# Kernel optimization log

Measured on AMD Instinct MI355X. Metric: run time of the kernel, lower is better.

Reference implementation:

```python
import jax, jax.numpy as jnp
import numpy as np

N = 32768          # total nodes in batch (M graphs * N_agents)
E = N * 8          # edges (k_neighbors = 8)
DIN = 16           # node_obs_dim
DE = 8             # edge_dim (rel_pos 2 + one-hot 4 + dist 1 + payoff 1)
HE = 128           # embed_hidden_size
C = 64             # TransformerConv out_channels
H = 4              # heads (concat)
HC = H * C         # 256, final node embedding dim
EPS = 1e-5


def _ln(x, g, b):
    m = x.mean(-1, keepdims=True)
    v = ((x - m) ** 2).mean(-1, keepdims=True)
    return (x - m) * jax.lax.rsqrt(v + EPS) * g + b


def _seg_softmax(s, seg, n):
    # numerically stable softmax over edges grouped by destination node
    m = jax.ops.segment_max(s, seg, num_segments=n)
    e = jnp.exp(s - m[seg])
    z = jax.ops.segment_sum(e, seg, num_segments=n)
    return e / z[seg]


def setup_inputs() -> dict:
    key = jax.random.key(0)
    ks = jax.random.split(key, 40)

    def w(i, shape):
        return jax.random.normal(ks[i], shape, jnp.float32) * 0.05

    inp = {
        "x": jax.random.normal(ks[0], (N, DIN), jnp.float32),
        "edge_index": jax.random.randint(ks[1], (2, E), 0, N, dtype=jnp.int32),
        "edge_attr": jax.random.normal(ks[2], (E, DE), jnp.float32),
        # EmbedConv: lin1 + LN + one hidden Linear + LN (embed_layer_N=1)
        "e_W1": w(3, (DIN + DE, HE)), "e_b1": jnp.zeros((HE,), jnp.float32),
        "e_g1": jnp.ones((HE,), jnp.float32), "e_be1": jnp.zeros((HE,), jnp.float32),
        "e_W2": w(4, (HE, HE)), "e_b2": jnp.zeros((HE,), jnp.float32),
        "e_g2": jnp.ones((HE,), jnp.float32), "e_be2": jnp.zeros((HE,), jnp.float32),
    }
    # Two TransformerConv layers; layer0 in=HE, layer1 in=HC (concat heads)
    for l, din in enumerate([HE, HC]):
        base = 5 + l * 6
        inp[f"l{l}_Wq"] = w(base, (din, HC));     inp[f"l{l}_bq"] = jnp.zeros((HC,), jnp.float32)
        inp[f"l{l}_Wk"] = w(base + 1, (din, HC)); inp[f"l{l}_bk"] = jnp.zeros((HC,), jnp.float32)
        inp[f"l{l}_Wv"] = w(base + 2, (din, HC)); inp[f"l{l}_bv"] = jnp.zeros((HC,), jnp.float32)
        inp[f"l{l}_We"] = w(base + 3, (DE, HC))   # lin_edge has no bias in PyG
        inp[f"l{l}_Ws"] = w(base + 4, (din, HC)); inp[f"l{l}_bs"] = jnp.zeros((HC,), jnp.float32)
    return inp


def _tconv(h, edge_attr, src, dst, Wq, bq, Wk, bk, Wv, bv, We, Ws, bs):
    q = (h @ Wq + bq).reshape(N, H, C)
    k = (h @ Wk + bk).reshape(N, H, C)
    v = (h @ Wv + bv).reshape(N, H, C)
    e = (edge_attr @ We).reshape(E, H, C)
    ke = k[src] + e                      # [E,H,C]
    ve = v[src] + e                      # [E,H,C]
    s = (q[dst] * ke).sum(-1) / np.float32(np.sqrt(C))  # [E,H]
    a = _seg_softmax(s, dst, N)          # softmax over in-edges of each dst
    out = jax.ops.segment_sum(a[..., None] * ve, dst, num_segments=N)
    return out.reshape(N, HC) + h @ Ws + bs  # root_weight skip + bias


def reference(x, edge_attr, e_W1, e_b1, e_g1, e_be1, e_W2, e_b2, e_g2, e_be2,
              l0_Wq, l0_bq, l0_Wk, l0_bk, l0_Wv, l0_bv, l0_We, l0_Ws, l0_bs,
              l1_Wq, l1_bq, l1_Wk, l1_bk, l1_Wv, l1_bv, l1_We, l1_Ws, l1_bs,
              edge_index):
    src, dst = edge_index[0], edge_index[1]
    # EmbedConv: per-edge MLP on cat(x_j, edge_attr), scatter-add to dst
    m = jnp.concatenate([x[src], edge_attr], axis=1)    # [E, DIN+DE]
    m = _ln(jax.nn.relu(m @ e_W1 + e_b1), e_g1, e_be1)
    m = _ln(jax.nn.relu(m @ e_W2 + e_b2), e_g2, e_be2)
    h = jax.ops.segment_sum(m, dst, num_segments=N)      # [N, HE]
    # Two TransformerConv layers with ReLU activations
    h = jax.nn.relu(_tconv(h, edge_attr, src, dst, l0_Wq, l0_bq, l0_Wk, l0_bk,
                           l0_Wv, l0_bv, l0_We, l0_Ws, l0_bs))
    h = jax.nn.relu(_tconv(h, edge_attr, src, dst, l1_Wq, l1_bq, l1_Wk, l1_bk,
                           l1_Wv, l1_bv, l1_We, l1_Ws, l1_bs))
    return h  # graph_aggr == 'node': [N, HC]
```

## Files before the change

### kernel.cpp

```cpp
#include <hip/hip_runtime.h>
#include <hip/hip_bf16.h>

#define NN 32768
#define NE 262144

typedef unsigned short u16;
typedef unsigned int   u32;
typedef __bf16 bf16x8 __attribute__((ext_vector_type(8)));
typedef float  f32x16 __attribute__((ext_vector_type(16)));

__device__ __forceinline__ float bf2f(u16 u){ return __uint_as_float(((u32)u)<<16); }
__device__ __forceinline__ u16 f2bf(float f){ __hip_bfloat16 h = __float2bfloat16(f); return *(u16*)&h; }
__device__ __forceinline__ float4 ldbf4(const u16* p){
  ushort4 u = *(const ushort4*)p;
  return make_float4(bf2f(u.x), bf2f(u.y), bf2f(u.z), bf2f(u.w));
}
__device__ __forceinline__ void gload16(const void* g, void* l){
  __builtin_amdgcn_global_load_lds(
      (const __attribute__((address_space(1))) void*)g,
      (__attribute__((address_space(3))) void*)l, 16, 0, 0);
}

__global__ void k_deg(const int* __restrict__ ei, int* deg){
  int e = blockIdx.x*256 + threadIdx.x;
  if (e < NE) atomicAdd(&deg[ei[NE + e]], 1);
}

__global__ void k_scan1(const int* __restrict__ deg, int* __restrict__ rowptr, int* __restrict__ bsum){
  const int t = threadIdx.x, b = blockIdx.x;
  const int i = b*256 + t;
  const int ln = t & 63, wv = t >> 6;
  int v = deg[i];
  #pragma unroll
  for (int d = 1; d < 64; d <<= 1){
    int u = __shfl_up(v, d, 64);
    if (ln >= d) v += u;
  }
  __shared__ int wsum[4];
  if (ln == 63) wsum[wv] = v;
  __syncthreads();
  int p = 0;
  #pragma unroll
  for (int w = 0; w < 4; w++) if (w < wv) p += wsum[w];
  v += p;
  rowptr[i + 1] = v;
  if (t == 255) bsum[b] = v;
}

__global__ void k_scan2(const int* __restrict__ bsum, int* __restrict__ boff){
  const int t = threadIdx.x;
  const int ln = t & 63, wv = t >> 6;
  int own = bsum[t];
  int v = own;
  #pragma unroll
  for (int d = 1; d < 64; d <<= 1){
    int u = __shfl_up(v, d, 64);
    if (ln >= d) v += u;
  }
  __shared__ int wsum[2];
  if (ln == 63) wsum[wv] = v;
  __syncthreads();
  if (wv == 1) v += wsum[0];
  boff[t] = v - own;
}

__global__ void k_scan3(int* __restrict__ rowptr, const int* __restrict__ boff){
  const int t = threadIdx.x, b = blockIdx.x;
  rowptr[1 + b*256 + t] += boff[b];
  if (b == 0 && t == 0) rowptr[0] = 0;
}

__global__ void k_fill(const int* __restrict__ ei, const int* __restrict__ rowptr,
                       int* cursor, int* __restrict__ csrc, int* __restrict__ cedge){
  int e = blockIdx.x*256 + threadIdx.x;
  if (e < NE){
    int d = ei[NE + e];
    int p = rowptr[d] + atomicAdd(&cursor[d], 1);
    csrc[p]  = ei[e];
    cedge[p] = e;
  }
}

__global__ void k_b2p(const float* __restrict__ W2, const float* __restrict__ be1,
                      const float* __restrict__ b2, float* __restrict__ b2p){
  int f = threadIdx.x;
  float a = b2[f];
  for (int k = 0; k < 128; k++) a += be1[k]*W2[k*128 + f];
  b2p[f] = a;
}

__global__ void k_eprep(const float* __restrict__ W1, const float* __restrict__ b1,
                        const float* __restrict__ W2, const float* __restrict__ g1,
                        const float* __restrict__ b2p, __bf16* __restrict__ Ecat){
  int i = blockIdx.x*256 + threadIdx.x;
  if (i >= 2816) return;
  bf16x8 v;
  if (i < 512){
    int r = i & 31, hh = (i>>5)&1, ks = (i>>6)&1, rt = i>>7;
    int feat = rt*32 + r, k0 = ks*16 + hh*8;
    #pragma unroll
    for (int j = 0; j < 8; j++){
      int k = k0 + j;
      float val = (k < 24) ? W1[k*128 + feat] : ((k == 24) ? b1[feat] : 0.f);
      v[j] = (__bf16)val;
    }
  } else {
    int m = i - 512;
    int r = m & 31, hh = (m>>5)&1, q = m>>6;
    int ks = q % 9, rt = q / 9;
    int feat = rt*32 + r, k0 = ks*16 + hh*8;
    #pragma unroll
    for (int j = 0; j < 8; j++){
      int k = k0 + j;
      float val = (k < 128) ? g1[k]*W2[k*128 + feat] : ((k == 128) ? b2p[feat] : 0.f);
      v[j] = (__bf16)val;
    }
  }
  *(bf16x8*)&Ecat[(size_t)i*8] = v;
}

struct WPtrs { const float* w[8]; const float* b[8]; };

__global__ void k_wprep(WPtrs wp, __bf16* __restrict__ W0cat, __bf16* __restrict__ W1cat,
                        float* __restrict__ bcat0, float* __restrict__ bcat1){
  int gid = blockIdx.x*256 + threadIdx.x;
  if (gid < 16384){
    int mat = gid >> 12, v = gid & 4095;
    int colm = v & 255, q = v >> 8;
    int k0 = (q>>1)*16 + (q&1)*8;
    const float* W = wp.w[mat];
    bf16x8 vec;
    #pragma unroll
    for (int j = 0; j < 8; j++) vec[j] = (__bf16)W[(size_t)(k0+j)*256 + colm];
    *(bf16x8*)&W0cat[((size_t)q*1024 + mat*256 + colm)*8] = vec;
  } else if (gid < 49152){
    int g = gid - 16384;
    int mat = g >> 13, v = g & 8191;
    int colm = v & 255, q = v >> 8;
    int k0 = (q>>1)*16 + (q&1)*8;
    const float* W = wp.w[4+mat];
    bf16x8 vec;
    #pragma unroll
    for (int j = 0; j < 8; j++) vec[j] = (__bf16)W[(size_t)(k0+j)*256 + colm];
    *(bf16x8*)&W1cat[((size_t)q*1024 + mat*256 + colm)*8] = vec;
  } else if (gid < 51200){
    int g = gid - 49152;
    if (g < 1024) bcat0[g] = wp.b[g>>8][g&255];
    else { int h = g-1024; bcat1[h] = wp.b[4 + (h>>8)][h&255]; }
  }
}

__global__ __launch_bounds__(256, 1) void k_embed(
    const float* __restrict__ x, const float* __restrict__ ea,
    const int* __restrict__ csrc, const int* __restrict__ cedge, const int* __restrict__ rowptr,
    const __bf16* __restrict__ Ecat,
    const float* __restrict__ g2, const float* __restrict__ be2,
    u16* __restrict__ h0b)
{
  __shared__ alignas(16) __bf16 sE[2816*8];
  __shared__ float sg2[128], sbe2[128];
  const int t = threadIdx.x;
  const int wv = t >> 6, ln = t & 63, hi = ln >> 5, c32 = ln & 31;

  #pragma unroll
  for (int k = 0; k < 11; k++){
    int base = k*256 + wv*64;
    gload16(Ecat + (size_t)(base + ln)*8, &sE[(size_t)base*8]);
  }
  if (t < 128){ sg2[t] = g2[t]; sbe2[t] = be2[t]; }
  asm volatile("s_waitcnt vmcnt(0)" ::: "memory");
  __syncthreads();

  const int d   = (blockIdx.x*4 + wv)*32 + c32;
  const int rp  = rowptr[d];
  const int deg = rowptr[d+1] - rp;
  int md = deg;
  #pragma unroll
  for (int m = 1; m < 32; m <<= 1) md = max(md, __shfl_xor(md, m, 32));

  f32x16 hacc[4] = {};

  bool vc = deg > 0;
  int p0 = vc ? rp : 0;
  int sc = csrc[p0], ec = cedge[p0];
  float4 xa = *(const float4*)&x[(size_t)sc*16 + hi*8];
  float4 xb = *(const float4*)&x[(size_t)sc*16 + hi*8 + 4];
  float4 ga = *(const float4*)&ea[(size_t)ec*8];
  float4 gb = *(const float4*)&ea[(size_t)ec*8 + 4];

  for (int j = 0; j < md; j++){
    const float vm = vc ? 1.f : 0.f;
    bf16x8 b1f0, b1f1;
    {
      float xv[8]; *(float4*)&xv[0] = xa; *(float4*)&xv[4] = xb;
      #pragma unroll
      for (int q = 0; q < 8; q++) b1f0[q] = (__bf16)(xv[q]*vm);
      float evv[8]; *(float4*)&evv[0] = ga; *(float4*)&evv[4] = gb;
      #pragma unroll
      for (int q = 0; q < 8; q++)
        b1f1[q] = (__bf16)(hi ? ((q == 0) ? vm : 0.f) : evv[q]*vm);
    }

    bool vn = (j + 1) < deg;
    int pn = vn ? (rp + j + 1) : 0;
    int sn = csrc[pn], en = cedge[pn];
    float4 xan = *(const float4*)&x[(size_t)sn*16 + hi*8];
    float4 xbn = *(const float4*)&x[(size_t)sn*16 + hi*8 + 4];
    float4 gan = *(const float4*)&ea[(size_t)en*8];
    float4 gbn = *(const float4*)&ea[(size_t)en*8 + 4];

    f32x16 a1[4] = {};
    #pragma unroll
    for (int ks = 0; ks < 2; ks++)
      #pragma unroll
      for (int rt = 0; rt < 4; rt++){
        bf16x8 af = *(const bf16x8*)&sE[((((rt*2 + ks)*2 + hi)*32) + c32)*8];
        a1[rt] = __builtin_amdgcn_mfma_f32_32x32x16_bf16(af, ks ? b1f1 : b1f0, a1[rt], 0, 0, 0);
      }

    {
      float s1 = 0.f, s2 = 0.f;
      #pragma unroll
      for (int rt = 0; rt < 4; rt++)
        #pragma unroll
        for (int rg = 0; rg < 16; rg++){
          float v = fmaxf(a1[rt][rg], 0.f);
          a1[rt][rg] = v; s1 += v; s2 += v*v;
        }
      s1 += __shfl_xor(s1, 32, 64);
      s2 += __shfl_xor(s2, 32, 64);
      float mean = s1*(1.f/128.f);
      float rs = rsqrtf(s2*(1.f/128.f) - mean*mean + 1e-5f);
      #pragma unroll
      for (int rt = 0; rt < 4; rt++)
        #pragma unroll
        for (int rg = 0; rg < 16; rg++)
          a1[rt][rg] = (a1[rt][rg] - mean)*rs;
    }

    f32x16 a2[4] = {};
    #pragma unroll
    for (int ks = 0; ks < 8; ks++){
      const int tt = ks >> 1, bb = (ks & 1)*8;
      float snd[4], rcv[4];
      #pragma unroll
      for (int q = 0; q < 4; q++)
        snd[q] = hi ? a1[tt][bb + q] : a1[tt][bb + 4 + q];
      #pragma unroll
      for (int q = 0; q < 4; q++)
        rcv[q] = __shfl_xor(snd[q], 32, 64);
      bf16x8 bf;
      #pragma unroll
      for (int q = 0; q < 4; q++){
        float lo = hi ? rcv[q] : a1[tt][bb + q];
        float hh = hi ? a1[tt][bb + 4 + q] : rcv[q];
        bf[q]     = (__bf16)lo;
        bf[4 + q] = (__bf16)hh;
      }
      #pragma unroll
      for (int rt = 0; rt < 4; rt++){
        bf16x8 af = *(const bf16x8*)&sE[(512 + (((rt*9 + ks)*2 + hi)*32) + c32)*8];
        a2[rt] = __builtin_amdgcn_mfma_f32_32x32x16_bf16(af, bf, a2[rt], 0, 0, 0);
      }
    }
    {
      bf16x8 bf;
      #pragma unroll
      for (int q = 0; q < 8; q++)
        bf[q] = (__bf16)((!hi && q == 0) ? vm : 0.f);
      #pragma unroll
      for (int rt = 0; rt < 4; rt++){
        bf16x8 af = *(const bf16x8*)&sE[(512 + (((rt*9 + 8)*2 + hi)*32) + c32)*8];
        a2[rt] = __builtin_amdgcn_mfma_f32_32x32x16_bf16(af, bf, a2[rt], 0, 0, 0);
      }
    }

    {
      float s1 = 0.f, s2 = 0.f;
      #pragma unroll
      for (int rt = 0; rt < 4; rt++)
        #pragma unroll
        for (int rg = 0; rg < 16; rg++){
          float v = fmaxf(a2[rt][rg], 0.f);
          a2[rt][rg] = v; s1 += v; s2 += v*v;
        }
      s1 += __shfl_xor(s1, 32, 64);
      s2 += __shfl_xor(s2, 32, 64);
      float mean = s1*(1.f/128.f);
      float rs = rsqrtf(s2*(1.f/128.f) - mean*mean + 1e-5f);
      #pragma unroll
      for (int rt = 0; rt < 4; rt++)
        #pragma unroll
        for (int rg = 0; rg < 16; rg++)
          hacc[rt][rg] += (a2[rt][rg] - mean)*rs;
    }

    vc = vn;
    xa = xan; xb = xbn; ga = gan; gb = gbn;
  }

  const float dd = (float)deg;
  #pragma unroll
  for (int rt = 0; rt < 4; rt++)
    #pragma unroll
    for (int q = 0; q < 4; q++){
      int fb = rt*32 + 8*q + 4*hi;
      ushort4 o;
      o.x = f2bf(sg2[fb+0]*hacc[rt][q*4+0] + dd*sbe2[fb+0]);
      o.y = f2bf(sg2[fb+1]*hacc[rt][q*4+1] + dd*sbe2[fb+1]);
      o.z = f2bf(sg2[fb+2]*hacc[rt][q*4+2] + dd*sbe2[fb+2]);
      o.w = f2bf(sg2[fb+3]*hacc[rt][q*4+3] + dd*sbe2[fb+3]);
      *(ushort4*)&h0b[(size_t)d*128 + fb] = o;
    }
}

template<int K>
__global__ __launch_bounds__(256) void k_qkvs2(const u16* __restrict__ A,
    const __bf16* __restrict__ Wcat, const float* __restrict__ bcat,
    u16* __restrict__ qo, u16* __restrict__ ko, u16* __restrict__ vo, u16* __restrict__ so)
{
  __shared__ alignas(16) __bf16 sA[1024*8];
  __shared__ alignas(16) __bf16 sB[1024*8];
  const int t = threadIdx.x;
  const int swz = (blockIdx.x & 7)*256 + (blockIdx.x >> 3);
  const int r0 = (swz >> 3)*128, c0 = (swz & 7)*128;
  const int wv = t >> 6, ln = t & 63, hi = ln >> 5, c32 = ln & 31;
  const int wr = wv >> 1, wc = wv & 1;

  f32x16 acc[2][2] = {};
  for (int kc = 0; kc < K/64; kc++){
    __syncthreads();
    #pragma unroll
    for (int ii = 0; ii < 4; ii++){
      int v = ii*256 + wv*64 + ln;
      int r = v & 31, hh = (v>>5)&1, ks = (v>>6)&3, rt = v>>8;
      const u16* src = A + (size_t)(r0 + rt*32 + r)*K + kc*64 + ks*16 + hh*8;
      gload16(src, &sA[(size_t)(ii*256 + wv*64)*8]);
    }
    #pragma unroll
    for (int ii = 0; ii < 4; ii++){
      int v = ii*256 + wv*64 + ln;
      int col = v & 127, q = v >> 7;
      const __bf16* src = Wcat + ((size_t)(kc*8 + q)*1024 + c0 + col)*8;
      gload16(src, &sB[(size_t)(ii*256 + wv*64)*8]);
    }
    asm volatile("s_waitcnt vmcnt(0)" ::: "memory");
    __syncthreads();
    #pragma unroll
    for (int ks = 0; ks < 4; ks++){
      bf16x8 af0 = *(const bf16x8*)&sA[((((wr*2+0)*4 + ks)*2 + hi)*32 + c32)*8];
      bf16x8 af1 = *(const bf16x8*)&sA[((((wr*2+1)*4 + ks)*2 + hi)*32 + c32)*8];
      bf16x8 bf0 = *(const bf16x8*)&sB[(((ks*2 + hi)*128) + wc*64 + c32)*8];
      bf16x8 bf1 = *(const bf16x8*)&sB[(((ks*2 + hi)*128) + wc*64 + 32 + c32)*8];
      acc[0][0] = __builtin_amdgcn_mfma_f32_32x32x16_bf16(af0, bf0, acc[0][0], 0, 0, 0);
      acc[0][1] = __builtin_amdgcn_mfma_f32_32x32x16_bf16(af0, bf1, acc[0][1], 0, 0, 0);
      acc[1][0] = __builtin_amdgcn_mfma_f32_32x32x16_bf16(af1, bf0, acc[1][0], 0, 0, 0);
      acc[1][1] = __builtin_amdgcn_mfma_f32_32x32x16_bf16(af1, bf1, acc[1][1], 0, 0, 0);
    }
  }

  u16* om = (c0 < 256) ? qo : (c0 < 512) ? ko : (c0 < 768) ? vo : so;
  const int cb = c0 & 255;
  #pragma unroll
  for (int ci = 0; ci < 2; ci++){
    int colm = cb + wc*64 + ci*32 + c32;
    float bb = bcat[c0 + wc*64 + ci*32 + c32];
    #pragma unroll
    for (int ri = 0; ri < 2; ri++){
      #pragma unroll
      for (int rg = 0; rg < 16; rg++){
        int row = r0 + (wr*2 + ri)*32 + (rg&3) + 8*(rg>>2) + 4*hi;
        om[(size_t)row*256 + colm] = f2bf(acc[ri][ci][rg] + bb);
      }
    }
  }
}

template<bool OBF>
__global__ __launch_bounds__(256) void k_attn(
    const int* __restrict__ csrc, const int* __restrict__ rowptr, const int* __restrict__ cedge,
    const float* __restrict__ ea, const float* __restrict__ We,
    const u16* __restrict__ qb, const u16* __restrict__ kb, const u16* __restrict__ vb,
    const u16* __restrict__ skb, void* __restrict__ outp)
{
  __shared__ float sWe[8*256];
  const int t = threadIdx.x;
  for (int i = t; i < 2048; i += 256) sWe[i] = We[i];
  __syncthreads();

  const int wv = t >> 6, ln = t & 63;
  const int f = (ln >> 4)*64 + (ln & 15)*4;
  const int gw = blockIdx.x*4 + wv, nW = gridDim.x*4;

  for (int d = gw; d < NN; d += nW){
    const int rp = rowptr[d];
    const int dg = rowptr[d+1] - rp;
    float4 qv = ldbf4(qb + (size_t)d*256 + f);
    qv.x *= 0.125f; qv.y *= 0.125f; qv.z *= 0.125f; qv.w *= 0.125f;
    float m = -INFINITY, l = 0.f, o0 = 0, o1 = 0, o2 = 0, o3 = 0;
    for (int j = 0; j < dg; j++){
      const int e = cedge[rp + j];
      const int s = csrc[rp + j];
      float eav[8];
      *(float4*)&eav[0] = *(const float4*)&ea[(size_t)e*8];
      *(float4*)&eav[4] = *(const float4*)&ea[(size_t)e*8 + 4];
      float e0 = 0, e1 = 0, e2 = 0, e3 = 0;
      #pragma unroll
      for (int i = 0; i < 8; i++){
        float4 w = *(const float4*)&sWe[i*256 + f];
        e0 += eav[i]*w.x; e1 += eav[i]*w.y; e2 += eav[i]*w.z; e3 += eav[i]*w.w;
      }
      float4 kv = ldbf4(kb + (size_t)s*256 + f);
      float sp = qv.x*(kv.x+e0) + qv.y*(kv.y+e1) + qv.z*(kv.z+e2) + qv.w*(kv.w+e3);
      sp += __shfl_xor(sp, 1, 64); sp += __shfl_xor(sp, 2, 64);
      sp += __shfl_xor(sp, 4, 64); sp += __shfl_xor(sp, 8, 64);
      float nm = fmaxf(m, sp);
      float sc = __expf(m - nm);
      float pp = __expf(sp - nm);
      l = l*sc + pp;
      float4 vv = ldbf4(vb + (size_t)s*256 + f);
      o0 = o0*sc + pp*(vv.x + e0);
      o1 = o1*sc + pp*(vv.y + e1);
      o2 = o2*sc + pp*(vv.z + e2);
      o3 = o3*sc + pp*(vv.w + e3);
      m = nm;
    }
    float il = (l > 0.f) ? 1.f/l : 0.f;
    float4 sv = ldbf4(skb + (size_t)d*256 + f);
    o0 = fmaxf(o0*il + sv.x, 0.f);
    o1 = fmaxf(o1*il + sv.y, 0.f);
    o2 = fmaxf(o2*il + sv.z, 0.f);
    o3 = fmaxf(o3*il + sv.w, 0.f);
    if constexpr (OBF){
      ushort4 o; o.x = f2bf(o0); o.y = f2bf(o1); o.z = f2bf(o2); o.w = f2bf(o3);
      *(ushort4*)((u16*)outp + (size_t)d*256 + f) = o;
    } else {
      *(float4*)((float*)outp + (size_t)d*256 + f) = make_float4(o0, o1, o2, o3);
    }
  }
}

extern "C" void kernel_launch(void* const* d_in, const int* in_sizes, int n_in,
                              void* d_out, int out_size, void* d_ws, size_t ws_size,
                              hipStream_t stream)
{
  (void)in_sizes; (void)n_in; (void)out_size; (void)ws_size;
  const float* x   = (const float*)d_in[0];
  const int*   ei  = (const int*)  d_in[1];
  const float* ea  = (const float*)d_in[2];
  const float* eW1 = (const float*)d_in[3];
  const float* eb1 = (const float*)d_in[4];
  const float* eg1 = (const float*)d_in[5];
  const float* ebe1= (const float*)d_in[6];
  const float* eW2 = (const float*)d_in[7];
  const float* eb2 = (const float*)d_in[8];
  const float* eg2 = (const float*)d_in[9];
  const float* ebe2= (const float*)d_in[10];

  char* ws = (char*)d_ws;
  const size_t MB = (size_t)1 << 20;
  const size_t KB = (size_t)1 << 10;
  int*   deg    = (int*)(ws);
  int*   cursor = (int*)(ws + 128*KB);
  int*   rowptr = (int*)(ws + 256*KB);
  int*   bsum   = (int*)(ws + 400*KB);
  int*   boff   = (int*)(ws + 402*KB);
  float* b2p    = (float*)(ws + 404*KB);
  int*   csrc   = (int*)(ws + 1*MB);
  int*   cedge  = (int*)(ws + 3*MB);
  u16*   qb     = (u16*)(ws + 20*MB);
  u16*   kbuf   = (u16*)(ws + 36*MB);
  u16*   vbuf   = (u16*)(ws + 52*MB);
  u16*   skb    = (u16*)(ws + 68*MB);
  u16*   h1     = (u16*)(ws + 84*MB);
  u16*   h0b    = (u16*)(ws + 100*MB);
  __bf16* W0cat = (__bf16*)(ws + 108*MB);
  __bf16* W1cat = (__bf16*)(ws + 109*MB);
  float* bcat0  = (float*)(ws + 110*MB);
  float* bcat1  = (float*)(ws + 110*MB + 64*KB);
  __bf16* Ecat  = (__bf16*)(ws + 111*MB);

  hipMemsetAsync(deg, 0, 256*KB, stream);

  k_deg  <<<NE/256, 256, 0, stream>>>(ei, deg);
  k_scan1<<<128,    256, 0, stream>>>(deg, rowptr, bsum);
  k_scan2<<<1,      128, 0, stream>>>(bsum, boff);
  k_scan3<<<128,    256, 0, stream>>>(rowptr, boff);
  k_fill <<<NE/256, 256, 0, stream>>>(ei, rowptr, cursor, csrc, cedge);
  k_b2p  <<<1,      128, 0, stream>>>(eW2, ebe1, eb2, b2p);
  k_eprep<<<11,     256, 0, stream>>>(eW1, eb1, eW2, eg1, b2p, Ecat);

  WPtrs wp;
  wp.w[0] = (const float*)d_in[11]; wp.b[0] = (const float*)d_in[12];
  wp.w[1] = (const float*)d_in[13]; wp.b[1] = (const float*)d_in[14];
  wp.w[2] = (const float*)d_in[15]; wp.b[2] = (const float*)d_in[16];
  wp.w[3] = (const float*)d_in[18]; wp.b[3] = (const float*)d_in[19];
  wp.w[4] = (const float*)d_in[20]; wp.b[4] = (const float*)d_in[21];
  wp.w[5] = (const float*)d_in[22]; wp.b[5] = (const float*)d_in[23];
  wp.w[6] = (const float*)d_in[24]; wp.b[6] = (const float*)d_in[25];
  wp.w[7] = (const float*)d_in[27]; wp.b[7] = (const float*)d_in[28];
  k_wprep<<<200, 256, 0, stream>>>(wp, W0cat, W1cat, bcat0, bcat1);

  k_embed<<<NN/128, 256, 0, stream>>>(x, ea, csrc, cedge, rowptr, Ecat, eg2, ebe2, h0b);

  k_qkvs2<128><<<2048, 256, 0, stream>>>(h0b, W0cat, bcat0, qb, kbuf, vbuf, skb);
  k_attn<true><<<NN/4, 256, 0, stream>>>(csrc, rowptr, cedge, ea, (const float*)d_in[17],
                                         qb, kbuf, vbuf, skb, (void*)h1);
  k_qkvs2<256><<<2048, 256, 0, stream>>>(h1, W1cat, bcat1, qb, kbuf, vbuf, skb);
  k_attn<false><<<NN/4, 256, 0, stream>>>(csrc, rowptr, cedge, ea, (const float*)d_in[26],
                                          qb, kbuf, vbuf, skb, d_out);
}
```

Baseline: 357.0 us.

## Store edge attributes in CSR order and prefetch next edge in attention

k_fill now copies each edge's attributes into a CSR-ordered buffer, so the embed and attention kernels read them contiguously and no longer gather through the cedge index. The attention loop also loads the next edge's source index, attributes, K and V before computing the current edge, to overlap memory latency with arithmetic. The cost is an extra 8MB write in k_fill and more live registers in the attention kernel.

```diff
diff --git a/kernel.cpp b/kernel.cpp
--- a/kernel.cpp
+++ b/kernel.cpp
@@ -71,13 +71,17 @@
 }
 
 __global__ void k_fill(const int* __restrict__ ei, const int* __restrict__ rowptr,
-                       int* cursor, int* __restrict__ csrc, int* __restrict__ cedge){
+                       int* cursor, const float* __restrict__ ea,
+                       int* __restrict__ csrc, float4* __restrict__ ea_csr){
   int e = blockIdx.x*256 + threadIdx.x;
   if (e < NE){
     int d = ei[NE + e];
     int p = rowptr[d] + atomicAdd(&cursor[d], 1);
-    csrc[p]  = ei[e];
-    cedge[p] = e;
+    csrc[p] = ei[e];
+    float4 a = *(const float4*)&ea[(size_t)e*8];
+    float4 b = *(const float4*)&ea[(size_t)e*8 + 4];
+    ea_csr[(size_t)p*2]     = a;
+    ea_csr[(size_t)p*2 + 1] = b;
   }
 }
 
@@ -151,8 +155,8 @@
 }
 
 __global__ __launch_bounds__(256, 1) void k_embed(
-    const float* __restrict__ x, const float* __restrict__ ea,
-    const int* __restrict__ csrc, const int* __restrict__ cedge, const int* __restrict__ rowptr,
+    const float* __restrict__ x, const float4* __restrict__ ea_csr,
+    const int* __restrict__ csrc, const int* __restrict__ rowptr,
     const __bf16* __restrict__ Ecat,
     const float* __restrict__ g2, const float* __restrict__ be2,
     u16* __restrict__ h0b)
@@ -182,11 +186,11 @@
 
   bool vc = deg > 0;
   int p0 = vc ? rp : 0;
-  int sc = csrc[p0], ec = cedge[p0];
+  int sc = csrc[p0];
   float4 xa = *(const float4*)&x[(size_t)sc*16 + hi*8];
   float4 xb = *(const float4*)&x[(size_t)sc*16 + hi*8 + 4];
-  float4 ga = *(const float4*)&ea[(size_t)ec*8];
-  float4 gb = *(const float4*)&ea[(size_t)ec*8 + 4];
+  float4 ga = ea_csr[(size_t)p0*2];
+  float4 gb = ea_csr[(size_t)p0*2 + 1];
 
   for (int j = 0; j < md; j++){
     const float vm = vc ? 1.f : 0.f;
@@ -203,11 +207,11 @@
 
     bool vn = (j + 1) < deg;
     int pn = vn ? (rp + j + 1) : 0;
-    int sn = csrc[pn], en = cedge[pn];
+    int sn = csrc[pn];
     float4 xan = *(const float4*)&x[(size_t)sn*16 + hi*8];
     float4 xbn = *(const float4*)&x[(size_t)sn*16 + hi*8 + 4];
-    float4 gan = *(const float4*)&ea[(size_t)en*8];
-    float4 gbn = *(const float4*)&ea[(size_t)en*8 + 4];
+    float4 gan = ea_csr[(size_t)pn*2];
+    float4 gbn = ea_csr[(size_t)pn*2 + 1];
 
     f32x16 a1[4] = {};
     #pragma unroll
@@ -378,8 +382,8 @@
 
 template<bool OBF>
 __global__ __launch_bounds__(256) void k_attn(
-    const int* __restrict__ csrc, const int* __restrict__ rowptr, const int* __restrict__ cedge,
-    const float* __restrict__ ea, const float* __restrict__ We,
+    const int* __restrict__ csrc, const int* __restrict__ rowptr,
+    const float4* __restrict__ ea_csr, const float* __restrict__ We,
     const u16* __restrict__ qb, const u16* __restrict__ kb, const u16* __restrict__ vb,
     const u16* __restrict__ skb, void* __restrict__ outp)
 {
@@ -398,33 +402,47 @@
     float4 qv = ldbf4(qb + (size_t)d*256 + f);
     qv.x *= 0.125f; qv.y *= 0.125f; qv.z *= 0.125f; qv.w *= 0.125f;
     float m = -INFINITY, l = 0.f, o0 = 0, o1 = 0, o2 = 0, o3 = 0;
-    for (int j = 0; j < dg; j++){
-      const int e = cedge[rp + j];
-      const int s = csrc[rp + j];
-      float eav[8];
-      *(float4*)&eav[0] = *(const float4*)&ea[(size_t)e*8];
-      *(float4*)&eav[4] = *(const float4*)&ea[(size_t)e*8 + 4];
-      float e0 = 0, e1 = 0, e2 = 0, e3 = 0;
-      #pragma unroll
-      for (int i = 0; i < 8; i++){
-        float4 w = *(const float4*)&sWe[i*256 + f];
-        e0 += eav[i]*w.x; e1 += eav[i]*w.y; e2 += eav[i]*w.z; e3 += eav[i]*w.w;
+
+    if (dg > 0){
+      int s0 = csrc[rp];
+      float4 ga = ea_csr[(size_t)rp*2];
+      float4 gb = ea_csr[(size_t)rp*2 + 1];
+      float4 kc = ldbf4(kb + (size_t)s0*256 + f);
+      float4 vc = ldbf4(vb + (size_t)s0*256 + f);
+
+      for (int j = 0; j < dg; j++){
+        int pn = rp + ((j + 1 < dg) ? (j + 1) : j);
+        int sn = csrc[pn];
+        float4 gan = ea_csr[(size_t)pn*2];
+        float4 gbn = ea_csr[(size_t)pn*2 + 1];
+        float4 kn = ldbf4(kb + (size_t)sn*256 + f);
+        float4 vn = ldbf4(vb + (size_t)sn*256 + f);
+
+        float eav[8];
+        *(float4*)&eav[0] = ga; *(float4*)&eav[4] = gb;
+        float e0 = 0, e1 = 0, e2 = 0, e3 = 0;
+        #pragma unroll
+        for (int i = 0; i < 8; i++){
+          float4 w = *(const float4*)&sWe[i*256 + f];
+          e0 += eav[i]*w.x; e1 += eav[i]*w.y; e2 += eav[i]*w.z; e3 += eav[i]*w.w;
+        }
+        float sp = qv.x*(kc.x+e0) + qv.y*(kc.y+e1) + qv.z*(kc.z+e2) + qv.w*(kc.w+e3);
+        sp += __shfl_xor(sp, 1, 64); sp += __shfl_xor(sp, 2, 64);
+        sp += __shfl_xor(sp, 4, 64); sp += __shfl_xor(sp, 8, 64);
+        float nm = fmaxf(m, sp);
+        float sc = __expf(m - nm);
+        float pp = __expf(sp - nm);
+        l = l*sc + pp;
+        o0 = o0*sc + pp*(vc.x + e0);
+        o1 = o1*sc + pp*(vc.y + e1);
+        o2 = o2*sc + pp*(vc.z + e2);
+        o3 = o3*sc + pp*(vc.w + e3);
+        m = nm;
+
+        kc = kn; vc = vn; ga = gan; gb = gbn;
       }
-      float4 kv = ldbf4(kb + (size_t)s*256 + f);
-      float sp = qv.x*(kv.x+e0) + qv.y*(kv.y+e1) + qv.z*(kv.z+e2) + qv.w*(kv.w+e3);
-      sp += __shfl_xor(sp, 1, 64); sp += __shfl_xor(sp, 2, 64);
-      sp += __shfl_xor(sp, 4, 64); sp += __shfl_xor(sp, 8, 64);
-      float nm = fmaxf(m, sp);
-      float sc = __expf(m - nm);
-      float pp = __expf(sp - nm);
-      l = l*sc + pp;
-      float4 vv = ldbf4(vb + (size_t)s*256 + f);
-      o0 = o0*sc + pp*(vv.x + e0);
-      o1 = o1*sc + pp*(vv.y + e1);
-      o2 = o2*sc + pp*(vv.z + e2);
-      o3 = o3*sc + pp*(vv.w + e3);
-      m = nm;
-    }
+    }
+
     float il = (l > 0.f) ? 1.f/l : 0.f;
     float4 sv = ldbf4(skb + (size_t)d*256 + f);
     o0 = fmaxf(o0*il + sv.x, 0.f);
@@ -467,7 +485,7 @@
   int*   boff   = (int*)(ws + 402*KB);
   float* b2p    = (float*)(ws + 404*KB);
   int*   csrc   = (int*)(ws + 1*MB);
-  int*   cedge  = (int*)(ws + 3*MB);
+  float4* ea_csr= (float4*)(ws + 4*MB);
   u16*   qb     = (u16*)(ws + 20*MB);
   u16*   kbuf   = (u16*)(ws + 36*MB);
   u16*   vbuf   = (u16*)(ws + 52*MB);
@@ -486,7 +504,7 @@
   k_scan1<<<128,    256, 0, stream>>>(deg, rowptr, bsum);
   k_scan2<<<1,      128, 0, stream>>>(bsum, boff);
   k_scan3<<<128,    256, 0, stream>>>(rowptr, boff);
-  k_fill <<<NE/256, 256, 0, stream>>>(ei, rowptr, cursor, csrc, cedge);
+  k_fill <<<NE/256, 256, 0, stream>>>(ei, rowptr, cursor, ea, csrc, ea_csr);
   k_b2p  <<<1,      128, 0, stream>>>(eW2, ebe1, eb2, b2p);
   k_eprep<<<11,     256, 0, stream>>>(eW1, eb1, eW2, eg1, b2p, Ecat);
 
@@ -501,12 +519,12 @@
   wp.w[7] = (const float*)d_in[27]; wp.b[7] = (const float*)d_in[28];
   k_wprep<<<200, 256, 0, stream>>>(wp, W0cat, W1cat, bcat0, bcat1);
 
-  k_embed<<<NN/128, 256, 0, stream>>>(x, ea, csrc, cedge, rowptr, Ecat, eg2, ebe2, h0b);
+  k_embed<<<NN/128, 256, 0, stream>>>(x, ea_csr, csrc, rowptr, Ecat, eg2, ebe2, h0b);
 
   k_qkvs2<128><<<2048, 256, 0, stream>>>(h0b, W0cat, bcat0, qb, kbuf, vbuf, skb);
-  k_attn<true><<<NN/4, 256, 0, stream>>>(csrc, rowptr, cedge, ea, (const float*)d_in[17],
+  k_attn<true><<<NN/4, 256, 0, stream>>>(csrc, rowptr, ea_csr, (const float*)d_in[17],
                                          qb, kbuf, vbuf, skb, (void*)h1);
   k_qkvs2<256><<<2048, 256, 0, stream>>>(h1, W1cat, bcat1, qb, kbuf, vbuf, skb);
-  k_attn<false><<<NN/4, 256, 0, stream>>>(csrc, rowptr, cedge, ea, (const float*)d_in[26],
+  k_attn<false><<<NN/4, 256, 0, stream>>>(csrc, rowptr, ea_csr, (const float*)d_in[26],
                                           qb, kbuf, vbuf, skb, d_out);
 }
```

New measurement: 335.8 us. -5.9%, faster.
